# Kernel optimization log

Measured on AMD Instinct MI355X. Metric: run time of the kernel, lower is better.

## Reference

```python
import jax, jax.numpy as jnp
import numpy as np
import math

B, S, DIM = 2, 2048, 1024
H, D = 16, 64  # num_head, head_dim; H*D == DIM

def setup_inputs() -> dict:
    key = jax.random.key(0)
    ks = jax.random.split(key, 10)
    s = 0.02
    return {
        "X": jax.random.normal(ks[0], (B, S, DIM), dtype=jnp.float32),
        "mask": jnp.ones((B, S), dtype=jnp.float32),
        "Wq": jax.random.normal(ks[1], (DIM, H * D), dtype=jnp.float32) * s,
        "bq": jnp.zeros((H * D,), dtype=jnp.float32),
        "Wk": jax.random.normal(ks[2], (DIM, H * D), dtype=jnp.float32) * s,
        "bk": jnp.zeros((H * D,), dtype=jnp.float32),
        "Wv": jax.random.normal(ks[3], (DIM, H * D), dtype=jnp.float32) * s,
        "bv": jnp.zeros((H * D,), dtype=jnp.float32),
        "Wo": jax.random.normal(ks[4], (H * D, DIM), dtype=jnp.float32) * s,
        "bo": jnp.zeros((DIM,), dtype=jnp.float32),
    }

def _split_heads(x):
    # [B, S, H*D] -> [B, H, S, D]
    b, s, _ = x.shape
    return x.reshape(b, s, H, D).transpose(0, 2, 1, 3)

def reference(X, mask, Wq, bq, Wk, bk, Wv, bv, Wo, bo):
    Q = _split_heads(X @ Wq + bq)
    K = _split_heads(X @ Wk + bk)
    V = _split_heads(X @ Wv + bv)
    # scaled dot-product attention with additive mask penalty
    dot = jnp.einsum('bhqd,bhkd->bhqk', Q, K) / math.sqrt(D)
    dot = dot - 1e6 * (1.0 - mask[:, None, None, :])
    attn = jax.nn.softmax(dot, axis=-1)
    ctx = jnp.einsum('bhqk,bhkd->bhqd', attn, V)
    # combine heads: [B, H, S, D] -> [B, S, H*D]
    ctx = ctx.transpose(0, 2, 1, 3).reshape(B, S, H * D)
    return ctx @ Wo + bo
```

## Files before the change

### kernel.cpp

```cpp
#include <hip/hip_runtime.h>
#include <cstdint>
#include <cstddef>

typedef __attribute__((ext_vector_type(8))) _Float16 f16x8;
typedef __attribute__((ext_vector_type(4))) _Float16 f16x4;
typedef __attribute__((ext_vector_type(4))) float f32x4;

#define MFMA_16x16x32(a, b, c) __builtin_amdgcn_mfma_f32_16x16x32_f16((a), (b), (c), 0, 0, 0)

static constexpr int kB = 2, kS = 2048, kDim = 1024, kH = 16, kD = 64;
static constexpr int kM = kB * kS;
static constexpr float kQScale = 0.125f * 1.44269504088896340736f;

__global__ void cvt_f32_to_f16(const float* __restrict__ in, _Float16* __restrict__ out, int n8) {
  int i = blockIdx.x * blockDim.x + threadIdx.x;
  if (i >= n8) return;
  const float4* p = (const float4*)in + (size_t)i * 2;
  float4 a = p[0], b = p[1];
  f16x8 h;
  h[0] = (_Float16)a.x; h[1] = (_Float16)a.y; h[2] = (_Float16)a.z; h[3] = (_Float16)a.w;
  h[4] = (_Float16)b.x; h[5] = (_Float16)b.y; h[6] = (_Float16)b.z; h[7] = (_Float16)b.w;
  ((f16x8*)out)[i] = h;
}

__global__ void transpose_cvt_w(const float* __restrict__ w0, const float* __restrict__ w1,
                                const float* __restrict__ w2, const float* __restrict__ w3,
                                _Float16* __restrict__ o0, _Float16* __restrict__ o1,
                                _Float16* __restrict__ o2, _Float16* __restrict__ o3) {
  const float* w; _Float16* o;
  switch (blockIdx.z) {
    case 0: w = w0; o = o0; break;
    case 1: w = w1; o = o1; break;
    case 2: w = w2; o = o2; break;
    default: w = w3; o = o3; break;
  }
  __shared__ alignas(16) _Float16 tile[64][72];
  const int kt = blockIdx.x * 64;
  const int nt = blockIdx.y * 64;
  const int tr = threadIdx.x >> 4;
  const int tc = threadIdx.x & 15;
#pragma unroll
  for (int rr = 0; rr < 4; ++rr) {
    int r = rr * 16 + tr;
    float4 v = *(const float4*)&w[(size_t)(kt + r) * kDim + nt + tc * 4];
    f16x4 hv;
    hv[0] = (_Float16)v.x; hv[1] = (_Float16)v.y; hv[2] = (_Float16)v.z; hv[3] = (_Float16)v.w;
    *(f16x4*)&tile[r][tc * 4] = hv;
  }
  __syncthreads();
#pragma unroll
  for (int rr = 0; rr < 4; ++rr) {
    int nl = rr * 16 + tr;
    f16x4 hv;
    hv[0] = tile[tc * 4 + 0][nl];
    hv[1] = tile[tc * 4 + 1][nl];
    hv[2] = tile[tc * 4 + 2][nl];
    hv[3] = tile[tc * 4 + 3][nl];
    *(f16x4*)&o[(size_t)(nt + nl) * kDim + kt + tc * 4] = hv;
  }
}

__global__ void mask_penalty(const float* __restrict__ mask, float* __restrict__ pen, int n) {
  int i = blockIdx.x * blockDim.x + threadIdx.x;
  if (i < n) pen[i] = -1.0e6f * (1.0f - mask[i]) * 1.44269504088896340736f;
}

__global__ __launch_bounds__(256, 2) void gemm_qkv(
    const _Float16* __restrict__ A,
    const _Float16* __restrict__ wt0, const _Float16* __restrict__ wt1, const _Float16* __restrict__ wt2,
    const float* __restrict__ bias0, const float* __restrict__ bias1, const float* __restrict__ bias2,
    _Float16* __restrict__ oq, _Float16* __restrict__ ok, _Float16* __restrict__ ov) {
  const _Float16* Bt; const float* bias; _Float16* out;
  switch (blockIdx.z) {
    case 0: Bt = wt0; bias = bias0; out = oq; break;
    case 1: Bt = wt1; bias = bias1; out = ok; break;
    default: Bt = wt2; bias = bias2; out = ov; break;
  }
  __shared__ alignas(16) _Float16 As[128 * 40];
  __shared__ alignas(16) _Float16 Bs[128 * 40];
  const int tid = threadIdx.x;
  const int lane = tid & 63;
  const int wave = tid >> 6;
  const int wm = wave & 1, wn = wave >> 1;
  const int l15 = lane & 15, quad = lane >> 4;
  const int m0 = blockIdx.x * 128, n0 = blockIdx.y * 128;

  const int r0 = tid >> 2;
  const int kc = (tid & 3) * 8;
  f32x4 acc[4][4] = {};

  for (int k0 = 0; k0 < kDim; k0 += 32) {
    __syncthreads();
    *(f16x8*)&As[r0 * 40 + kc]        = *(const f16x8*)&A[(size_t)(m0 + r0) * kDim + k0 + kc];
    *(f16x8*)&As[(r0 + 64) * 40 + kc] = *(const f16x8*)&A[(size_t)(m0 + r0 + 64) * kDim + k0 + kc];
    *(f16x8*)&Bs[r0 * 40 + kc]        = *(const f16x8*)&Bt[(size_t)(n0 + r0) * kDim + k0 + kc];
    *(f16x8*)&Bs[(r0 + 64) * 40 + kc] = *(const f16x8*)&Bt[(size_t)(n0 + r0 + 64) * kDim + k0 + kc];
    __syncthreads();
    f16x8 af[4], bf[4];
#pragma unroll
    for (int t = 0; t < 4; ++t) af[t] = *(const f16x8*)&As[(wm * 64 + t * 16 + l15) * 40 + quad * 8];
#pragma unroll
    for (int t = 0; t < 4; ++t) bf[t] = *(const f16x8*)&Bs[(wn * 64 + t * 16 + l15) * 40 + quad * 8];
#pragma unroll
    for (int i = 0; i < 4; ++i)
#pragma unroll
      for (int j = 0; j < 4; ++j)
        acc[i][j] = MFMA_16x16x32(af[i], bf[j], acc[i][j]);
  }

  const int mbase = m0 + wm * 64 + quad * 4;
  const int nbase = n0 + wn * 64 + l15;
  if (blockIdx.z == 2) {
#pragma unroll
    for (int j = 0; j < 4; ++j) {
      int n = nbase + j * 16;
      float bv = bias[n];
      int h = n >> 6, d = n & 63;
#pragma unroll
      for (int i = 0; i < 4; ++i) {
        int m = mbase + i * 16;
        int b = m >> 11, s = m & (kS - 1);
        f16x4 hv;
#pragma unroll
        for (int r = 0; r < 4; ++r) hv[r] = (_Float16)(acc[i][j][r] + bv);
        *(f16x4*)&out[((size_t)((b * kH + h) * kD + d)) * kS + s] = hv;
      }
    }
  } else {
    const float osc = (blockIdx.z == 0) ? kQScale : 1.0f;
#pragma unroll
    for (int j = 0; j < 4; ++j) {
      int n = nbase + j * 16;
      float bv = bias[n];
      int h = n >> 6, d = n & 63;
#pragma unroll
      for (int i = 0; i < 4; ++i) {
        int mrow = mbase + i * 16;
#pragma unroll
        for (int r = 0; r < 4; ++r) {
          int m = mrow + r;
          int b = m >> 11, s = m & (kS - 1);
          out[(size_t)(((b * kH + h) * kS) + s) * kD + d] = (_Float16)((acc[i][j][r] + bv) * osc);
        }
      }
    }
  }
}

__global__ __launch_bounds__(256, 3) void attn(
    const _Float16* __restrict__ Q, const _Float16* __restrict__ K,
    const _Float16* __restrict__ V, const float* __restrict__ pen2,
    _Float16* __restrict__ ctx) {
  const int bh = blockIdx.y;
  const int b = bh >> 4;
  const int q0 = blockIdx.x * 128;
  const int tid = threadIdx.x, lane = tid & 63, wave = tid >> 6;
  const int l15 = lane & 15, quad = lane >> 4;

  __shared__ alignas(16) _Float16 Ks[128 * 72];
  __shared__ alignas(16) _Float16 Vs[64 * 136];
  __shared__ alignas(16) _Float16 Ps[4][16 * 136];
  __shared__ float pens[128];

  const _Float16* Qh = Q + (size_t)bh * kS * kD;
  const _Float16* Kh = K + (size_t)bh * kS * kD;
  const _Float16* Vh = V + (size_t)bh * kS * kD;

  f16x8 qf[2][2];
#pragma unroll
  for (int t = 0; t < 2; ++t) {
    int qrow = q0 + wave * 32 + t * 16 + l15;
#pragma unroll
    for (int kk = 0; kk < 2; ++kk)
      qf[t][kk] = *(const f16x8*)&Qh[(size_t)qrow * kD + kk * 32 + quad * 8];
  }

  f32x4 o_acc[2][4] = {};
  float l_part[2][4] = {};

  for (int kb = 0; kb < kS; kb += 128) {
    __syncthreads();
#pragma unroll
    for (int i = 0; i < 4; ++i) {
      int c = tid + 256 * i;
      int row = c >> 3, dc = (c & 7) * 8;
      *(f16x8*)&Ks[row * 72 + dc] = *(const f16x8*)&Kh[(size_t)(kb + row) * kD + dc];
    }
#pragma unroll
    for (int i = 0; i < 4; ++i) {
      int c = tid + 256 * i;
      int row = c >> 4, sc8 = (c & 15) * 8;
      *(f16x8*)&Vs[row * 136 + sc8] = *(const f16x8*)&Vh[(size_t)row * kS + kb + sc8];
    }
    if (tid < 128) pens[tid] = pen2[b * kS + kb + tid];
    __syncthreads();

#pragma unroll
    for (int t = 0; t < 2; ++t) {
      f32x4 s_acc[8] = {};
#pragma unroll
      for (int kk = 0; kk < 2; ++kk)
#pragma unroll
        for (int col = 0; col < 8; ++col) {
          f16x8 kf = *(const f16x8*)&Ks[(col * 16 + l15) * 72 + kk * 32 + quad * 8];
          s_acc[col] = MFMA_16x16x32(qf[t][kk], kf, s_acc[col]);
        }

#pragma unroll
      for (int col = 0; col < 8; ++col) {
        float pn = pens[col * 16 + l15];
#pragma unroll
        for (int r = 0; r < 4; ++r) {
          float pv = __builtin_exp2f(s_acc[col][r] + pn);
          l_part[t][r] += pv;
          Ps[wave][(quad * 4 + r) * 136 + col * 16 + l15] = (_Float16)pv;
        }
      }

#pragma unroll
      for (int ks = 0; ks < 4; ++ks) {
        f16x8 pf = *(const f16x8*)&Ps[wave][l15 * 136 + ks * 32 + quad * 8];
#pragma unroll
        for (int c = 0; c < 4; ++c) {
          f16x8 vf = *(const f16x8*)&Vs[(c * 16 + l15) * 136 + ks * 32 + quad * 8];
          o_acc[t][c] = MFMA_16x16x32(pf, vf, o_acc[t][c]);
        }
      }
    }
  }

  const int h = bh & 15;
#pragma unroll
  for (int t = 0; t < 2; ++t)
#pragma unroll
    for (int r = 0; r < 4; ++r) {
      float lsum = l_part[t][r];
#pragma unroll
      for (int off = 1; off < 16; off <<= 1) lsum += __shfl_xor(lsum, off, 64);
      float inv = 1.0f / lsum;
      int s = q0 + wave * 32 + t * 16 + quad * 4 + r;
#pragma unroll
      for (int c = 0; c < 4; ++c) {
        int d = c * 16 + l15;
        ctx[((size_t)(b * kS + s)) * kDim + h * kD + d] = (_Float16)(o_acc[t][c][r] * inv);
      }
    }
}

__global__ __launch_bounds__(256, 2) void gemm_out(
    const _Float16* __restrict__ A, const _Float16* __restrict__ Bt,
    const float* __restrict__ bias, float* __restrict__ out) {
  __shared__ alignas(16) _Float16 As[128 * 40];
  __shared__ alignas(16) _Float16 Bs[128 * 40];
  const int tid = threadIdx.x;
  const int lane = tid & 63;
  const int wave = tid >> 6;
  const int wm = wave & 1, wn = wave >> 1;
  const int l15 = lane & 15, quad = lane >> 4;
  const int m0 = blockIdx.x * 128, n0 = blockIdx.y * 128;

  const int r0 = tid >> 2;
  const int kc = (tid & 3) * 8;
  f32x4 acc[4][4] = {};

  for (int k0 = 0; k0 < kDim; k0 += 32) {
    __syncthreads();
    *(f16x8*)&As[r0 * 40 + kc]        = *(const f16x8*)&A[(size_t)(m0 + r0) * kDim + k0 + kc];
    *(f16x8*)&As[(r0 + 64) * 40 + kc] = *(const f16x8*)&A[(size_t)(m0 + r0 + 64) * kDim + k0 + kc];
    *(f16x8*)&Bs[r0 * 40 + kc]        = *(const f16x8*)&Bt[(size_t)(n0 + r0) * kDim + k0 + kc];
    *(f16x8*)&Bs[(r0 + 64) * 40 + kc] = *(const f16x8*)&Bt[(size_t)(n0 + r0 + 64) * kDim + k0 + kc];
    __syncthreads();
    f16x8 af[4], bf[4];
#pragma unroll
    for (int t = 0; t < 4; ++t) af[t] = *(const f16x8*)&As[(wm * 64 + t * 16 + l15) * 40 + quad * 8];
#pragma unroll
    for (int t = 0; t < 4; ++t) bf[t] = *(const f16x8*)&Bs[(wn * 64 + t * 16 + l15) * 40 + quad * 8];
#pragma unroll
    for (int i = 0; i < 4; ++i)
#pragma unroll
      for (int j = 0; j < 4; ++j)
        acc[i][j] = MFMA_16x16x32(af[i], bf[j], acc[i][j]);
  }

  const int mbase = m0 + wm * 64 + quad * 4;
  const int nbase = n0 + wn * 64 + l15;
#pragma unroll
  for (int j = 0; j < 4; ++j) {
    int n = nbase + j * 16;
    float bv = bias[n];
#pragma unroll
    for (int i = 0; i < 4; ++i) {
      int mrow = mbase + i * 16;
#pragma unroll
      for (int r = 0; r < 4; ++r)
        out[(size_t)(mrow + r) * kDim + n] = acc[i][j][r] + bv;
    }
  }
}

extern "C" void kernel_launch(void* const* d_in, const int* in_sizes, int n_in,
                              void* d_out, int out_size, void* d_ws, size_t ws_size,
                              hipStream_t stream) {
  (void)in_sizes; (void)n_in; (void)out_size; (void)ws_size;
  const float* X    = (const float*)d_in[0];
  const float* mask = (const float*)d_in[1];
  const float* Wq   = (const float*)d_in[2];
  const float* bq   = (const float*)d_in[3];
  const float* Wk   = (const float*)d_in[4];
  const float* bk   = (const float*)d_in[5];
  const float* Wv   = (const float*)d_in[6];
  const float* bv   = (const float*)d_in[7];
  const float* Wo   = (const float*)d_in[8];
  const float* bo   = (const float*)d_in[9];
  float* out = (float*)d_out;

  char* ws = (char*)d_ws;
  _Float16* Xh   = (_Float16*)(ws);
  _Float16* Wqt  = (_Float16*)(ws + ((size_t)8  << 20));
  _Float16* Wkt  = (_Float16*)(ws + ((size_t)10 << 20));
  _Float16* Wvt  = (_Float16*)(ws + ((size_t)12 << 20));
  _Float16* Wot  = (_Float16*)(ws + ((size_t)14 << 20));
  _Float16* Qh   = (_Float16*)(ws + ((size_t)16 << 20));
  _Float16* Kh   = (_Float16*)(ws + ((size_t)24 << 20));
  _Float16* Vh   = (_Float16*)(ws + ((size_t)32 << 20));
  _Float16* Ch   = (_Float16*)(ws + ((size_t)40 << 20));
  float*    pen2 = (float*)   (ws + ((size_t)48 << 20));

  cvt_f32_to_f16<<<dim3(kM * kDim / 8 / 256), dim3(256), 0, stream>>>(X, Xh, kM * kDim / 8);
  transpose_cvt_w<<<dim3(16, 16, 4), dim3(256), 0, stream>>>(Wq, Wk, Wv, Wo, Wqt, Wkt, Wvt, Wot);
  mask_penalty<<<dim3(16), dim3(256), 0, stream>>>(mask, pen2, kB * kS);
  gemm_qkv<<<dim3(32, 8, 3), dim3(256), 0, stream>>>(Xh, Wqt, Wkt, Wvt, bq, bk, bv, Qh, Kh, Vh);
  attn<<<dim3(16, 32), dim3(256), 0, stream>>>(Qh, Kh, Vh, pen2, Ch);
  gemm_out<<<dim3(32, 8), dim3(256), 0, stream>>>(Ch, Wot, bo, out);
}
```

Measured before the change: 239.4 us.

## Widen GEMM K-tile to 64 and transpose attention score layout for vector P/ctx stores

Both GEMM kernels now stage 64-wide K slices per iteration instead of 32, halving the number of barrier pairs per output tile at the cost of more LDS. The attention kernel swaps MFMA operand order so scores come out transposed (keys along the accumulator rows), which allows penalties to be read as vectors, P to be written as f16x4 instead of scalar stores, fewer shuffles in the row-sum reduction, and vectorized ctx stores. K fragments are shared across both query subtiles, and attention occupancy hint drops from 3 to 2 blocks because the P buffer doubles.

```diff
diff --git a/kernel.cpp b/kernel.cpp
--- a/kernel.cpp
+++ b/kernel.cpp
@@ -76,8 +76,8 @@
     case 1: Bt = wt1; bias = bias1; out = ok; break;
     default: Bt = wt2; bias = bias2; out = ov; break;
   }
-  __shared__ alignas(16) _Float16 As[128 * 40];
-  __shared__ alignas(16) _Float16 Bs[128 * 40];
+  __shared__ alignas(16) _Float16 As[128 * 72];
+  __shared__ alignas(16) _Float16 Bs[128 * 72];
   const int tid = threadIdx.x;
   const int lane = tid & 63;
   const int wave = tid >> 6;
@@ -85,27 +85,31 @@
   const int l15 = lane & 15, quad = lane >> 4;
   const int m0 = blockIdx.x * 128, n0 = blockIdx.y * 128;
 
-  const int r0 = tid >> 2;
-  const int kc = (tid & 3) * 8;
   f32x4 acc[4][4] = {};
 
-  for (int k0 = 0; k0 < kDim; k0 += 32) {
-    __syncthreads();
-    *(f16x8*)&As[r0 * 40 + kc]        = *(const f16x8*)&A[(size_t)(m0 + r0) * kDim + k0 + kc];
-    *(f16x8*)&As[(r0 + 64) * 40 + kc] = *(const f16x8*)&A[(size_t)(m0 + r0 + 64) * kDim + k0 + kc];
-    *(f16x8*)&Bs[r0 * 40 + kc]        = *(const f16x8*)&Bt[(size_t)(n0 + r0) * kDim + k0 + kc];
-    *(f16x8*)&Bs[(r0 + 64) * 40 + kc] = *(const f16x8*)&Bt[(size_t)(n0 + r0 + 64) * kDim + k0 + kc];
-    __syncthreads();
-    f16x8 af[4], bf[4];
-#pragma unroll
-    for (int t = 0; t < 4; ++t) af[t] = *(const f16x8*)&As[(wm * 64 + t * 16 + l15) * 40 + quad * 8];
-#pragma unroll
-    for (int t = 0; t < 4; ++t) bf[t] = *(const f16x8*)&Bs[(wn * 64 + t * 16 + l15) * 40 + quad * 8];
-#pragma unroll
-    for (int i = 0; i < 4; ++i)
-#pragma unroll
-      for (int j = 0; j < 4; ++j)
-        acc[i][j] = MFMA_16x16x32(af[i], bf[j], acc[i][j]);
+  for (int k0 = 0; k0 < kDim; k0 += 64) {
+    __syncthreads();
+#pragma unroll
+    for (int i = 0; i < 4; ++i) {
+      int c = tid + 256 * i;
+      int row = c >> 3, kc = (c & 7) * 8;
+      *(f16x8*)&As[row * 72 + kc] = *(const f16x8*)&A[(size_t)(m0 + row) * kDim + k0 + kc];
+      *(f16x8*)&Bs[row * 72 + kc] = *(const f16x8*)&Bt[(size_t)(n0 + row) * kDim + k0 + kc];
+    }
+    __syncthreads();
+#pragma unroll
+    for (int kk = 0; kk < 2; ++kk) {
+      f16x8 af[4], bf[4];
+#pragma unroll
+      for (int t = 0; t < 4; ++t) af[t] = *(const f16x8*)&As[(wm * 64 + t * 16 + l15) * 72 + kk * 32 + quad * 8];
+#pragma unroll
+      for (int t = 0; t < 4; ++t) bf[t] = *(const f16x8*)&Bs[(wn * 64 + t * 16 + l15) * 72 + kk * 32 + quad * 8];
+#pragma unroll
+      for (int i = 0; i < 4; ++i)
+#pragma unroll
+        for (int j = 0; j < 4; ++j)
+          acc[i][j] = MFMA_16x16x32(af[i], bf[j], acc[i][j]);
+    }
   }
 
   const int mbase = m0 + wm * 64 + quad * 4;
@@ -147,7 +151,7 @@
   }
 }
 
-__global__ __launch_bounds__(256, 3) void attn(
+__global__ __launch_bounds__(256, 2) void attn(
     const _Float16* __restrict__ Q, const _Float16* __restrict__ K,
     const _Float16* __restrict__ V, const float* __restrict__ pen2,
     _Float16* __restrict__ ctx) {
@@ -159,8 +163,8 @@
 
   __shared__ alignas(16) _Float16 Ks[128 * 72];
   __shared__ alignas(16) _Float16 Vs[64 * 136];
-  __shared__ alignas(16) _Float16 Ps[4][16 * 136];
-  __shared__ float pens[128];
+  __shared__ alignas(16) _Float16 Pt[4][32 * 136];
+  __shared__ alignas(16) float pens[128];
 
   const _Float16* Qh = Q + (size_t)bh * kS * kD;
   const _Float16* Kh = K + (size_t)bh * kS * kD;
@@ -176,7 +180,7 @@
   }
 
   f32x4 o_acc[2][4] = {};
-  float l_part[2][4] = {};
+  float l_part[2] = {0.0f, 0.0f};
 
   for (int kb = 0; kb < kS; kb += 128) {
     __syncthreads();
@@ -195,63 +199,68 @@
     if (tid < 128) pens[tid] = pen2[b * kS + kb + tid];
     __syncthreads();
 
+    f32x4 s[2][8] = {};
+#pragma unroll
+    for (int kk = 0; kk < 2; ++kk)
+#pragma unroll
+      for (int colt = 0; colt < 8; ++colt) {
+        f16x8 kf = *(const f16x8*)&Ks[(colt * 16 + l15) * 72 + kk * 32 + quad * 8];
+        s[0][colt] = MFMA_16x16x32(kf, qf[0][kk], s[0][colt]);
+        s[1][colt] = MFMA_16x16x32(kf, qf[1][kk], s[1][colt]);
+      }
+
 #pragma unroll
     for (int t = 0; t < 2; ++t) {
-      f32x4 s_acc[8] = {};
-#pragma unroll
-      for (int kk = 0; kk < 2; ++kk)
-#pragma unroll
-        for (int col = 0; col < 8; ++col) {
-          f16x8 kf = *(const f16x8*)&Ks[(col * 16 + l15) * 72 + kk * 32 + quad * 8];
-          s_acc[col] = MFMA_16x16x32(qf[t][kk], kf, s_acc[col]);
+#pragma unroll
+      for (int colt = 0; colt < 8; ++colt) {
+        f32x4 pn = *(const f32x4*)&pens[colt * 16 + quad * 4];
+        f16x4 ph;
+#pragma unroll
+        for (int r = 0; r < 4; ++r) {
+          float pv = __builtin_exp2f(s[t][colt][r] + pn[r]);
+          l_part[t] += pv;
+          ph[r] = (_Float16)pv;
         }
-
-#pragma unroll
-      for (int col = 0; col < 8; ++col) {
-        float pn = pens[col * 16 + l15];
-#pragma unroll
-        for (int r = 0; r < 4; ++r) {
-          float pv = __builtin_exp2f(s_acc[col][r] + pn);
-          l_part[t][r] += pv;
-          Ps[wave][(quad * 4 + r) * 136 + col * 16 + l15] = (_Float16)pv;
-        }
-      }
-
-#pragma unroll
-      for (int ks = 0; ks < 4; ++ks) {
-        f16x8 pf = *(const f16x8*)&Ps[wave][l15 * 136 + ks * 32 + quad * 8];
-#pragma unroll
-        for (int c = 0; c < 4; ++c) {
-          f16x8 vf = *(const f16x8*)&Vs[(c * 16 + l15) * 136 + ks * 32 + quad * 8];
-          o_acc[t][c] = MFMA_16x16x32(pf, vf, o_acc[t][c]);
-        }
+        *(f16x4*)&Pt[wave][(t * 16 + l15) * 136 + colt * 16 + quad * 4] = ph;
+      }
+    }
+
+#pragma unroll
+    for (int ks = 0; ks < 4; ++ks) {
+      f16x8 pf0 = *(const f16x8*)&Pt[wave][(l15) * 136 + ks * 32 + quad * 8];
+      f16x8 pf1 = *(const f16x8*)&Pt[wave][(16 + l15) * 136 + ks * 32 + quad * 8];
+#pragma unroll
+      for (int c = 0; c < 4; ++c) {
+        f16x8 vf = *(const f16x8*)&Vs[(c * 16 + l15) * 136 + ks * 32 + quad * 8];
+        o_acc[0][c] = MFMA_16x16x32(vf, pf0, o_acc[0][c]);
+        o_acc[1][c] = MFMA_16x16x32(vf, pf1, o_acc[1][c]);
       }
     }
   }
 
   const int h = bh & 15;
 #pragma unroll
-  for (int t = 0; t < 2; ++t)
-#pragma unroll
-    for (int r = 0; r < 4; ++r) {
-      float lsum = l_part[t][r];
-#pragma unroll
-      for (int off = 1; off < 16; off <<= 1) lsum += __shfl_xor(lsum, off, 64);
-      float inv = 1.0f / lsum;
-      int s = q0 + wave * 32 + t * 16 + quad * 4 + r;
-#pragma unroll
-      for (int c = 0; c < 4; ++c) {
-        int d = c * 16 + l15;
-        ctx[((size_t)(b * kS + s)) * kDim + h * kD + d] = (_Float16)(o_acc[t][c][r] * inv);
-      }
-    }
+  for (int t = 0; t < 2; ++t) {
+    float lsum = l_part[t];
+    lsum += __shfl_xor(lsum, 16, 64);
+    lsum += __shfl_xor(lsum, 32, 64);
+    float inv = 1.0f / lsum;
+    int q = q0 + wave * 32 + t * 16 + l15;
+#pragma unroll
+    for (int c = 0; c < 4; ++c) {
+      f16x4 oh;
+#pragma unroll
+      for (int r = 0; r < 4; ++r) oh[r] = (_Float16)(o_acc[t][c][r] * inv);
+      *(f16x4*)&ctx[((size_t)(b * kS + q)) * kDim + h * kD + c * 16 + quad * 4] = oh;
+    }
+  }
 }
 
 __global__ __launch_bounds__(256, 2) void gemm_out(
     const _Float16* __restrict__ A, const _Float16* __restrict__ Bt,
     const float* __restrict__ bias, float* __restrict__ out) {
-  __shared__ alignas(16) _Float16 As[128 * 40];
-  __shared__ alignas(16) _Float16 Bs[128 * 40];
+  __shared__ alignas(16) _Float16 As[128 * 72];
+  __shared__ alignas(16) _Float16 Bs[128 * 72];
   const int tid = threadIdx.x;
   const int lane = tid & 63;
   const int wave = tid >> 6;
@@ -259,27 +268,31 @@
   const int l15 = lane & 15, quad = lane >> 4;
   const int m0 = blockIdx.x * 128, n0 = blockIdx.y * 128;
 
-  const int r0 = tid >> 2;
-  const int kc = (tid & 3) * 8;
   f32x4 acc[4][4] = {};
 
-  for (int k0 = 0; k0 < kDim; k0 += 32) {
-    __syncthreads();
-    *(f16x8*)&As[r0 * 40 + kc]        = *(const f16x8*)&A[(size_t)(m0 + r0) * kDim + k0 + kc];
-    *(f16x8*)&As[(r0 + 64) * 40 + kc] = *(const f16x8*)&A[(size_t)(m0 + r0 + 64) * kDim + k0 + kc];
-    *(f16x8*)&Bs[r0 * 40 + kc]        = *(const f16x8*)&Bt[(size_t)(n0 + r0) * kDim + k0 + kc];
-    *(f16x8*)&Bs[(r0 + 64) * 40 + kc] = *(const f16x8*)&Bt[(size_t)(n0 + r0 + 64) * kDim + k0 + kc];
-    __syncthreads();
-    f16x8 af[4], bf[4];
-#pragma unroll
-    for (int t = 0; t < 4; ++t) af[t] = *(const f16x8*)&As[(wm * 64 + t * 16 + l15) * 40 + quad * 8];
-#pragma unroll
-    for (int t = 0; t < 4; ++t) bf[t] = *(const f16x8*)&Bs[(wn * 64 + t * 16 + l15) * 40 + quad * 8];
-#pragma unroll
-    for (int i = 0; i < 4; ++i)
-#pragma unroll
-      for (int j = 0; j < 4; ++j)
-        acc[i][j] = MFMA_16x16x32(af[i], bf[j], acc[i][j]);
+  for (int k0 = 0; k0 < kDim; k0 += 64) {
+    __syncthreads();
+#pragma unroll
+    for (int i = 0; i < 4; ++i) {
+      int c = tid + 256 * i;
+      int row = c >> 3, kc = (c & 7) * 8;
+      *(f16x8*)&As[row * 72 + kc] = *(const f16x8*)&A[(size_t)(m0 + row) * kDim + k0 + kc];
+      *(f16x8*)&Bs[row * 72 + kc] = *(const f16x8*)&Bt[(size_t)(n0 + row) * kDim + k0 + kc];
+    }
+    __syncthreads();
+#pragma unroll
+    for (int kk = 0; kk < 2; ++kk) {
+      f16x8 af[4], bf[4];
+#pragma unroll
+      for (int t = 0; t < 4; ++t) af[t] = *(const f16x8*)&As[(wm * 64 + t * 16 + l15) * 72 + kk * 32 + quad * 8];
+#pragma unroll
+      for (int t = 0; t < 4; ++t) bf[t] = *(const f16x8*)&Bs[(wn * 64 + t * 16 + l15) * 72 + kk * 32 + quad * 8];
+#pragma unroll
+      for (int i = 0; i < 4; ++i)
+#pragma unroll
+        for (int j = 0; j < 4; ++j)
+          acc[i][j] = MFMA_16x16x32(af[i], bf[j], acc[i][j]);
+    }
   }
 
   const int mbase = m0 + wm * 64 + quad * 4;
```

Result: faster. 219.7 us (-8.3%).
